# Kernel tuning notes

Hardware: AMD Instinct MI355X
Metric: run time of the kernel (lower is better)

The kernel has to match this reference:

```python
import jax, jax.numpy as jnp
import numpy as np

N_HEAD, D_HEAD = 10, 38
D_MODEL, D_INNER = 380, 900
QLEN, BSZ = 1024, 4
MIN_LEN, MAX_LEN = -1024, 1024
EPS = 1e-5
SCALE = 1.0 / D_HEAD ** 0.5


def _ln(x, g, b):
    m = x.mean(-1, keepdims=True)
    v = ((x - m) ** 2).mean(-1, keepdims=True)
    return (x - m) / jnp.sqrt(v + EPS) * g + b


def setup_inputs() -> dict:
    key = jax.random.key(0)
    ks = jax.random.split(key, 10)
    s = 0.02
    w = jax.random.normal(ks[0], (QLEN, BSZ, D_MODEL), jnp.float32)
    # sinusoidal relative position embeddings over positions max_len .. min_len
    pos = jnp.arange(MAX_LEN, MIN_LEN - 1, -1, dtype=jnp.float32)  # [rlen]
    inv_freq = 1.0 / (10000.0 ** (jnp.arange(0, D_MODEL, 2, dtype=jnp.float32) / D_MODEL))
    sin_inp = pos[:, None] * inv_freq[None, :]
    r = jnp.concatenate([jnp.sin(sin_inp), jnp.cos(sin_inp)], axis=-1)  # [rlen, d_model]
    # causal mask, True = attend; layout [qlen, klen, bsz]
    attn_mask = jnp.broadcast_to(jnp.tril(jnp.ones((QLEN, QLEN), bool))[:, :, None], (QLEN, QLEN, BSZ))
    attn_relpos = jax.random.randint(ks[1], (BSZ, QLEN, QLEN), MIN_LEN, MAX_LEN + 1).astype(jnp.int32)
    return {
        'w': w,
        'r': r,
        'r_w_bias': s * jax.random.normal(ks[2], (N_HEAD, D_HEAD), jnp.float32),
        'r_r_bias': s * jax.random.normal(ks[3], (N_HEAD, D_HEAD), jnp.float32),
        'qkv_w': s * jax.random.normal(ks[4], (3 * N_HEAD * D_HEAD, D_MODEL), jnp.float32),
        'r_w': s * jax.random.normal(ks[5], (N_HEAD * D_HEAD, D_MODEL), jnp.float32),
        'o_w': s * jax.random.normal(ks[6], (D_MODEL, N_HEAD * D_HEAD), jnp.float32),
        'ln1_g': jnp.ones(D_MODEL, jnp.float32), 'ln1_b': jnp.zeros(D_MODEL, jnp.float32),
        'ff_w1': s * jax.random.normal(ks[7], (D_INNER, D_MODEL), jnp.float32),
        'ff_b1': jnp.zeros(D_INNER, jnp.float32),
        'ff_w2': s * jax.random.normal(ks[8], (D_MODEL, D_INNER), jnp.float32),
        'ff_b2': jnp.zeros(D_MODEL, jnp.float32),
        'ln2_g': jnp.ones(D_MODEL, jnp.float32), 'ln2_b': jnp.zeros(D_MODEL, jnp.float32),
        'attn_mask': attn_mask,
        'attn_relpos': attn_relpos,
        'min_len': MIN_LEN,
        'max_len': MAX_LEN,
    }


def reference(w, r, r_w_bias, r_r_bias, qkv_w, r_w, o_w, ln1_g, ln1_b,
              ff_w1, ff_b1, ff_w2, ff_b2, ln2_g, ln2_b,
              attn_mask, attn_relpos, min_len, max_len):
    qlen, bsz, _ = w.shape
    # qkv projection (no mems, post-lnorm)
    heads = jnp.einsum('ibm,hm->ibh', w, qkv_w)  # [q, b, 3*nh*dh]
    q, k, v = jnp.split(heads, 3, axis=-1)
    q = q.reshape(qlen, bsz, N_HEAD, D_HEAD)
    k = k.reshape(qlen, bsz, N_HEAD, D_HEAD)
    v = v.reshape(qlen, bsz, N_HEAD, D_HEAD)
    rk = (r @ r_w.T).reshape(-1, N_HEAD, D_HEAD)  # [rlen, nh, dh]
    # content score AC and position score BD (Transformer-XL)
    AC = jnp.einsum('ibnd,jbnd->ijbn', q + r_w_bias, k)   # [q, k, b, n]
    BD = jnp.einsum('ibnd,jnd->ijbn', q + r_r_bias, rk)   # [q, rlen, b, n]
    # gather-based relative position indexing (attn_relpos path)
    idx = (max_len - jnp.clip(attn_relpos, min_len, max_len)).transpose(1, 2, 0)  # [q, k, b]
    idx4 = jnp.broadcast_to(idx[..., None], idx.shape + (N_HEAD,))
    BD = jnp.take_along_axis(BD, idx4, axis=1)            # [q, k, b, n]
    score = (AC + BD) * SCALE
    score = jnp.where(attn_mask[:, :, :, None], score, -jnp.inf)
    prob = jax.nn.softmax(score, axis=1)
    vec = jnp.einsum('ijbn,jbnd->ibnd', prob, v).reshape(qlen, bsz, N_HEAD * D_HEAD)
    attn_out = vec @ o_w.T
    out = _ln(w + attn_out, ln1_g, ln1_b)
    # position-wise FF, post-lnorm
    core = jax.nn.relu(out @ ff_w1.T + ff_b1) @ ff_w2.T + ff_b2
    return _ln(out + core, ln2_g, ln2_b)
```

## Files before the change

kernel.cpp:

```cpp
#include <hip/hip_runtime.h>
#include <math.h>

#define QLEN 1024
#define BSZ 4
#define NH 10
#define DH 38
#define DM 380
#define DI 900
#define H3 1140
#define RLEN 2049
#define RLP 2112
#define RLD 2052
#define SCALE 0.16222142113076254f

typedef unsigned short ushortt;
typedef unsigned char uchar;
typedef __attribute__((ext_vector_type(8))) short short8;
typedef __attribute__((ext_vector_type(4))) float float4v;

__device__ __forceinline__ float bf2f(ushortt u) {
    return __uint_as_float(((unsigned int)u) << 16);
}
__device__ __forceinline__ ushortt f2bf(float f) {
    unsigned int u = __float_as_uint(f);
    u += 0x7fffu + ((u >> 16) & 1u);
    return (ushortt)(u >> 16);
}
__device__ __forceinline__ uchar f2e4m3(float f) {
    unsigned u = __float_as_uint(f);
    unsigned s = (u >> 24) & 0x80u;
    unsigned b = u & 0x7fffffffu;
    b += 0x7FFFFu + ((b >> 20) & 1u);
    int E = (int)(b >> 23) - 120;
    if (E <= 0) return (uchar)s;
    if (E > 15 || (E == 15 && ((b >> 20) & 7u) > 6u)) return (uchar)(s | 0x7Eu);
    return (uchar)(s | ((unsigned)E << 3) | ((b >> 20) & 7u));
}
__device__ __forceinline__ float e4m32f(uchar v) {
    unsigned s = ((unsigned)(v & 0x80u)) << 24;
    int E = (v >> 3) & 15; unsigned m = v & 7u;
    if (E == 0) return __uint_as_float(s);
    return __uint_as_float(s | ((unsigned)(E + 120) << 23) | (m << 20));
}

__device__ __forceinline__ void convseg(const float* src, ushortt* dst,
                                        int R, int C, int Rp, int Cp,
                                        int tid0, int stride) {
    const int total = Rp * Cp;
    for (int i = tid0; i < total; i += stride) {
        int r = i / Cp, c = i - r * Cp;
        float v = (r < R && c < C) ? src[(size_t)r * C + c] : 0.f;
        dst[i] = f2bf(v);
    }
}

__global__ __launch_bounds__(256)
void prep_all(const float* __restrict__ w,    ushortt* __restrict__ w_bf,
              const float* __restrict__ qkv,  ushortt* __restrict__ qkv_bf,
              const float* __restrict__ r,    ushortt* __restrict__ r_bf,
              const float* __restrict__ rw,   ushortt* __restrict__ rw_bf,
              const float* __restrict__ ow,   ushortt* __restrict__ ow_bf,
              const float* __restrict__ f1,   ushortt* __restrict__ f1_bf,
              const float* __restrict__ f2,   ushortt* __restrict__ f2_bf,
              ushortt* __restrict__ qw_bf, ushortt* __restrict__ Kb, ushortt* __restrict__ Vb,
              ushortt* __restrict__ qr_bf, ushortt* __restrict__ rk_bf,
              ushortt* __restrict__ vec) {
    const int stride = gridDim.x * 256;
    const int tid0 = blockIdx.x * 256 + threadIdx.x;
    convseg(w,   w_bf,   4096, DM, 4096, 384, tid0, stride);
    convseg(qkv, qkv_bf, H3,   DM, 1152, 384, tid0, stride);
    convseg(r,   r_bf,   RLEN, DM, 2176, 384, tid0, stride);
    convseg(rw,  rw_bf,  DM,   DM, 384,  384, tid0, stride);
    convseg(ow,  ow_bf,  DM,   DM, 384,  384, tid0, stride);
    convseg(f1,  f1_bf,  DI,   DM, 960,  384, tid0, stride);
    convseg(f2,  f2_bf,  DM,   DI, 384,  928, tid0, stride);
    for (int i = tid0; i < BSZ * NH * 1024 * 2; i += stride) {
        size_t idx = (size_t)(i >> 1) * 40 + 38 + (i & 1);
        qw_bf[idx] = 0; Kb[idx] = 0; Vb[idx] = 0;
    }
    for (int i = tid0; i < 4096 * 4; i += stride)
        vec[(size_t)(i >> 2) * 384 + 380 + (i & 3)] = 0;
    for (int i = tid0; i < BSZ * NH * 1024 * 26; i += stride) {
        int row = i / 26, c = 38 + i % 26;
        qr_bf[(size_t)row * 64 + c] = 0;
    }
    for (int i = tid0; i < NH * RLP * 26; i += stride) {
        int row = i / 26, c = 38 + i % 26;
        rk_bf[(size_t)row * 64 + c] = 0;
    }
    for (int i = tid0; i < NH * 63 * 64; i += stride) {
        int n = i / (63 * 64), rem = i % (63 * 64);
        rk_bf[((size_t)n * RLP + RLEN + rem / 64) * 64 + rem % 64] = 0;
    }
}

template<int EPI>
__global__ __launch_bounds__(256)
void gemm_mfma(const ushortt* __restrict__ A, const ushortt* __restrict__ B,
               const float* __restrict__ bias, void* __restrict__ Cout,
               int M, int N, int Kpp, int ldc,
               const float* __restrict__ bias2, float* __restrict__ out2,
               float* __restrict__ out3, float* __restrict__ out4) {
    __shared__ __align__(16) ushortt As[128 * 32];
    __shared__ __align__(16) ushortt Bs[64 * 32];
    const int tid = threadIdx.x;
    const int wid = tid >> 6, lane = tid & 63;
    const int bRow = blockIdx.y * 128, bCol = blockIdx.x * 64;

    float4v acc[2][4];
    const float4v zz = {0.f, 0.f, 0.f, 0.f};
    #pragma unroll
    for (int m = 0; m < 2; ++m)
        #pragma unroll
        for (int n = 0; n < 4; ++n) acc[m][n] = zz;

    const int arow = tid >> 1, acol = (tid & 1) * 16;
    const int brow = tid >> 2, bcol = (tid & 3) * 8;
    const int fr = lane & 15, kg = lane >> 4;

    for (int k0 = 0; k0 < Kpp; k0 += 32) {
        const ushortt* ag = A + (size_t)(bRow + arow) * Kpp + k0 + acol;
        float4v a0 = *(const float4v*)ag;
        float4v a1 = *(const float4v*)(ag + 8);
        const ushortt* bg = B + (size_t)(bCol + brow) * Kpp + k0 + bcol;
        float4v b0 = *(const float4v*)bg;
        __syncthreads();
        *(float4v*)&As[arow * 32 + acol] = a0;
        *(float4v*)&As[arow * 32 + acol + 8] = a1;
        *(float4v*)&Bs[brow * 32 + bcol] = b0;
        __syncthreads();

        short8 bf[4];
        #pragma unroll
        for (int n = 0; n < 4; ++n)
            bf[n] = *(const short8*)&Bs[(n * 16 + fr) * 32 + kg * 8];
        #pragma unroll
        for (int m = 0; m < 2; ++m) {
            short8 af = *(const short8*)&As[(wid * 32 + m * 16 + fr) * 32 + kg * 8];
            #pragma unroll
            for (int n = 0; n < 4; ++n)
                acc[m][n] = __builtin_amdgcn_mfma_f32_16x16x32_bf16(af, bf[n], acc[m][n], 0, 0, 0);
        }
    }

    #pragma unroll
    for (int m = 0; m < 2; ++m)
        #pragma unroll
        for (int n = 0; n < 4; ++n)
            #pragma unroll
            for (int j = 0; j < 4; ++j) {
                const int row = bRow + wid * 32 + m * 16 + (lane >> 4) * 4 + j;
                const int col = bCol + n * 16 + (lane & 15);
                const float v = acc[m][n][j];
                if (EPI == 0) {
                    if (row < M && col < N) ((float*)Cout)[(size_t)row * ldc + col] = v;
                } else if (EPI == 3) {
                    if (row < M && col < 928) {
                        float h = (col < DI) ? fmaxf(v + bias[col], 0.f) : 0.f;
                        ((ushortt*)Cout)[(size_t)row * 928 + col] = f2bf(h);
                    }
                } else if (EPI == 4) {
                    if (row < M && col < N) ((float*)Cout)[(size_t)row * ldc + col] = v + bias[col];
                } else if (EPI == 5) {
                    if (col < H3) {
                        int part = col / 380;
                        int c = col - part * 380;
                        int nh = c / 38, d = c - nh * 38;
                        int q = row >> 2, b2 = row & 3;
                        size_t i40 = (((size_t)b2 * NH + nh) * 1024 + q) * 40 + d;
                        size_t i64 = (((size_t)b2 * NH + nh) * 1024 + q) * 64 + d;
                        if (part == 0) {
                            ((ushortt*)Cout)[i40] = f2bf(v + bias[c]);
                            ((ushortt*)out2)[i64] = f2bf(v + bias2[c]);
                        } else if (part == 1) ((ushortt*)out3)[i40] = f2bf(v);
                        else ((ushortt*)out4)[i40] = f2bf(v);
                    }
                } else {
                    if (row < RLEN && col < DM) {
                        int nh = col / 38, d = col - nh * 38;
                        ((ushortt*)Cout)[((size_t)nh * RLP + row) * 64 + d] = f2bf(v);
                    }
                }
            }
}

__global__ __launch_bounds__(256)
void bd_gemm(const ushortt* __restrict__ qr, const ushortt* __restrict__ rk,
             uchar* __restrict__ BD, int bofs, int nb) {
    __shared__ __align__(16) ushortt As[64][72];
    __shared__ __align__(16) ushortt Bs[32][72];
    __shared__ __align__(16) uchar Call[64 * 32 * 10];
    const int bid = blockIdx.x;
    const int xcd = bid & 7, t = bid >> 3;
    const int gl = t / 65, jt = t - gl * 65;
    const int G = gl * 8 + xcd;
    const int lb = G >> 4, qt = G & 15;
    const int tid = threadIdx.x;
    const int wid = tid >> 6, lane = tid & 63;
    const int j0 = jt * 32, q0 = qt * 64;
    const int fr = lane & 15, kg = lane >> 4;
    const int jcount = min(32, RLEN - j0);

    for (int n = 0; n < NH; ++n) {
        const ushortt* Ab = qr + (((size_t)(bofs + lb) * NH + n) * 1024 + q0) * 64;
        const ushortt* Bb = rk + ((size_t)n * RLP + j0) * 64;
        __syncthreads();
        {
            int rr = tid >> 2, cc = (tid & 3) * 16;
            *(float4v*)&As[rr][cc] = *(const float4v*)(Ab + (size_t)rr * 64 + cc);
            *(float4v*)&As[rr][cc + 8] = *(const float4v*)(Ab + (size_t)rr * 64 + cc + 8);
            int br = tid >> 3, bc = (tid & 7) * 8;
            *(float4v*)&Bs[br][bc] = *(const float4v*)(Bb + (size_t)br * 64 + bc);
        }
        __syncthreads();
        float4v acc[2] = {{0.f,0.f,0.f,0.f},{0.f,0.f,0.f,0.f}};
        #pragma unroll
        for (int ks = 0; ks < 64; ks += 32) {
            short8 af = *(const short8*)&As[wid * 16 + fr][ks + kg * 8];
            #pragma unroll
            for (int c = 0; c < 2; ++c) {
                short8 bfr = *(const short8*)&Bs[c * 16 + fr][ks + kg * 8];
                acc[c] = __builtin_amdgcn_mfma_f32_16x16x32_bf16(af, bfr, acc[c], 0, 0, 0);
            }
        }
        #pragma unroll
        for (int c = 0; c < 2; ++c)
            #pragma unroll
            for (int jj = 0; jj < 4; ++jj) {
                int rq = wid * 16 + (lane >> 4) * 4 + jj;
                int cj = c * 16 + (lane & 15);
                Call[(rq * 32 + cj) * 10 + n] = f2e4m3(acc[c][jj]);
            }
    }
    __syncthreads();
    if (jcount == 32) {
        const unsigned* Cdw = (const unsigned*)Call;
        unsigned* G2 = (unsigned*)BD;
        for (int idx = tid; idx < 64 * 80; idx += 256) {
            int rr = idx / 80, rem = idx - rr * 80;
            size_t gdw = (((size_t)(lb * 1024 + q0 + rr) * RLD + j0) * 10) >> 2;
            G2[gdw + rem] = Cdw[rr * 80 + rem];
        }
    } else {
        for (int idx = tid; idx < 64 * 10; idx += 256) {
            int rr = idx / 10, n2 = idx - rr * 10;
            BD[((size_t)(lb * 1024 + q0 + rr) * RLD + j0) * 10 + n2] = Call[rr * 320 + n2];
        }
    }
}

__global__ __launch_bounds__(256)
void attn7(const ushortt* __restrict__ qwb, const ushortt* __restrict__ Kp,
           const ushortt* __restrict__ Vp, const uchar* __restrict__ BD,
           const int* __restrict__ relpos,
           ushortt* __restrict__ op, float2* __restrict__ ml, int b0, int nb) {
    const int bid = blockIdx.x;
    const int xcd = bid & 7, t = bid >> 3;
    const int gl = t / 10, n = t - gl * 10;
    const int G = gl * 8 + xcd;
    int qc, lb, s;
    {
        const int c3 = 32 * nb, c2 = 24 * nb, c1 = 16 * nb;
        if (G < c3)                { qc = 31 - G / (4 * nb); int r2 = G % (4 * nb); lb = r2 >> 2; s = r2 & 3; }
        else if (G < c3 + c2)      { int l2 = G - c3; qc = 23 - l2 / (3 * nb); int r2 = l2 % (3 * nb); lb = r2 / 3; s = r2 % 3; }
        else if (G < c3 + c2 + c1) { int l2 = G - c3 - c2; qc = 15 - l2 / (2 * nb); int r2 = l2 % (2 * nb); lb = r2 >> 1; s = r2 & 1; }
        else                       { int l2 = G - c3 - c2 - c1; qc = 7 - l2 / nb; lb = l2 % nb; s = 0; }
    }
    const int ns = (qc >> 3) + 1;
    const int qbase = qc * 32;
    const int b = b0 + lb;
    const int tid = threadIdx.x;
    const int wid = tid >> 6, lane = tid & 63;
    const int row = tid >> 3, kg = tid & 7;
    const int qi = qbase + row;
    const size_t bn = (size_t)b * NH + n;
    const size_t prow = ((size_t)s * (BSZ * NH) + bn) * 1024 + qi;
    const int ntiles = (qbase + 95) >> 6;

    __shared__ __align__(16) ushortt KtL[64 * 48];
    __shared__ __align__(16) ushortt VtL[64 * 40];
    __shared__ __align__(16) ushortt qwL[32 * 48];
    __shared__ __align__(16) ushortt sL[32 * 66];

    const ushortt* Kbase = Kp + bn * 1024 * 40;
    const ushortt* Vbase = Vp + bn * 1024 * 40;
    const int fr = lane & 15;
    const int kg8 = (lane >> 4) * 8;
    const bool kgz = (lane >> 4) == 0;
    const short8 z8 = {0, 0, 0, 0, 0, 0, 0, 0};

    for (int e = tid; e < 160; e += 256) {
        int rr = e / 5, cc = (e % 5) * 8;
        *(short8*)&qwL[rr * 48 + cc] = *(const short8*)(qwb + (bn * 1024 + qbase + rr) * 40 + cc);
    }
    float o[5] = {0.f, 0.f, 0.f, 0.f, 0.f};
    float mrun = -INFINITY, lrun = 0.f;
    const int* rp = relpos + ((size_t)b * QLEN + qi) * QLEN;
    const uchar* bdrow = BD + ((size_t)(lb * 1024 + qi)) * (RLD * 10) + n;

    for (int kt = s; kt < ntiles; kt += ns) {
        const int k0 = kt * 64;
        __syncthreads();
        for (int e = tid; e < 320; e += 256) {
            int rr = e / 5, cc = (e % 5) * 8;
            *(short8*)&KtL[rr * 48 + cc] = *(const short8*)(Kbase + (size_t)(k0 + rr) * 40 + cc);
        }
        for (int e = tid; e < 320; e += 256)
            ((short8*)VtL)[e] = ((const short8*)(Vbase + (size_t)k0 * 40))[e];
        __syncthreads();

        int jv[8];
        #pragma unroll
        for (int ss = 0; ss < 8; ++ss) {
            const int kk = k0 + kg + ss * 8;
            int j = -1;
            if (kk <= qi) {
                int rpv = rp[kk];
                rpv = rpv < -1024 ? -1024 : (rpv > 1024 ? 1024 : rpv);
                j = 1024 - rpv;
            }
            jv[ss] = j;
        }
        float bdv[8];
        #pragma unroll
        for (int ss = 0; ss < 8; ++ss)
            bdv[ss] = (jv[ss] >= 0) ? e4m32f(bdrow[(size_t)jv[ss] * 10]) : 0.f;

        {
            const int mt = wid >> 1, ctb = (wid & 1) * 2;
            short8 a0 = *(const short8*)&qwL[(mt * 16 + fr) * 48 + kg8];
            short8 a1 = kgz ? *(const short8*)&qwL[(mt * 16 + fr) * 48 + 32] : z8;
            #pragma unroll
            for (int c = 0; c < 2; ++c) {
                const int ct = ctb + c;
                short8 b0f = *(const short8*)&KtL[(ct * 16 + fr) * 48 + kg8];
                short8 b1f = kgz ? *(const short8*)&KtL[(ct * 16 + fr) * 48 + 32] : z8;
                float4v acc = {0.f, 0.f, 0.f, 0.f};
                acc = __builtin_amdgcn_mfma_f32_16x16x32_bf16(a0, b0f, acc, 0, 0, 0);
                acc = __builtin_amdgcn_mfma_f32_16x16x32_bf16(a1, b1f, acc, 0, 0, 0);
                #pragma unroll
                for (int j = 0; j < 4; ++j)
                    sL[(mt * 16 + (lane >> 4) * 4 + j) * 66 + ct * 16 + fr] = f2bf(acc[j]);
            }
        }
        __syncthreads();

        float sarr[8];
        float pmax = -INFINITY;
        #pragma unroll
        for (int ss = 0; ss < 8; ++ss) {
            float sv = -INFINITY;
            if (jv[ss] >= 0)
                sv = (bf2f(sL[row * 66 + kg + ss * 8]) + bdv[ss]) * SCALE;
            sarr[ss] = sv;
            pmax = fmaxf(pmax, sv);
        }
        pmax = fmaxf(pmax, __shfl_xor(pmax, 1, 64));
        pmax = fmaxf(pmax, __shfl_xor(pmax, 2, 64));
        pmax = fmaxf(pmax, __shfl_xor(pmax, 4, 64));
        const float nm = fmaxf(mrun, pmax);
        const float corr = __expf(mrun - nm);
        float psum = 0.f;
        ushortt* prw = sL + row * 66;
        #pragma unroll
        for (int ss = 0; ss < 8; ++ss) {
            float p = __expf(sarr[ss] - nm);
            psum += p;
            prw[kg + ss * 8] = f2bf(p);
        }
        psum += __shfl_xor(psum, 1, 64);
        psum += __shfl_xor(psum, 2, 64);
        psum += __shfl_xor(psum, 4, 64);
        lrun = lrun * corr + psum;
        mrun = nm;
        #pragma unroll
        for (int jj = 0; jj < 5; ++jj) o[jj] *= corr;
        int kmax = qi - k0 + 1; if (kmax > 64) kmax = 64;
        #pragma unroll 4
        for (int k = 0; k < kmax; ++k) {
            float p = bf2f(prw[k]);
            const ushortt* vr = VtL + k * 40;
            uint2 v4u = *(const uint2*)(vr + 4 * kg);
            o[0] += p * bf2f((ushortt)(v4u.x & 0xffff));
            o[1] += p * bf2f((ushortt)(v4u.x >> 16));
            o[2] += p * bf2f((ushortt)(v4u.y & 0xffff));
            o[3] += p * bf2f((ushortt)(v4u.y >> 16));
            o[4] += p * bf2f(vr[32 + kg]);
        }
    }
    ushortt* oprow = op + prow * 40;
    #pragma unroll
    for (int jj = 0; jj < 4; ++jj) oprow[4 * kg + jj] = f2bf(o[jj]);
    oprow[32 + kg] = f2bf(o[4]);
    if (kg == 0) ml[prow] = make_float2(mrun, lrun);
}

__global__ __launch_bounds__(256)
void attn_combine(const ushortt* __restrict__ op, const float2* __restrict__ ml,
                  ushortt* __restrict__ vec) {
    const int idx = blockIdx.x * 256 + threadIdx.x;
    if (idx >= BSZ * NH * 1024 * 38) return;
    const int d = idx % 38;
    const int rh = idx / 38;
    const int q = rh & 1023;
    const int bn = rh >> 10;
    const int b = bn / NH, n = bn - b * NH;
    const int ns = ((q >> 5) >> 3) + 1;
    const size_t stride = (size_t)BSZ * NH * 1024;
    float M = -INFINITY;
    float2 mv[4];
    for (int sp = 0; sp < ns; ++sp) {
        mv[sp] = ml[sp * stride + rh];
        M = fmaxf(M, mv[sp].x);
    }
    float l = 0.f, o = 0.f;
    for (int sp = 0; sp < ns; ++sp) {
        float w = __expf(mv[sp].x - M);
        l += mv[sp].y * w;
        o += bf2f(op[(sp * stride + rh) * 40 + d]) * w;
    }
    vec[((size_t)q * BSZ + b) * 384 + (size_t)n * 38 + d] = f2bf(o / l);
}

template<bool WRITE_BF>
__global__ __launch_bounds__(256)
void ln_kernel(const float* __restrict__ x1, const float* __restrict__ x2,
               const float* __restrict__ g, const float* __restrict__ bb,
               float* __restrict__ outf, ushortt* __restrict__ outbf) {
    const int row = blockIdx.x;
    const float* p1 = x1 + (size_t)row * DM;
    const float* p2 = x2 + (size_t)row * DM;
    __shared__ float xb[DM];
    __shared__ float red[256];
    const int tid = threadIdx.x;
    float s = 0.f;
    for (int i = tid; i < DM; i += 256) { float v = p1[i] + p2[i]; xb[i] = v; s += v; }
    red[tid] = s; __syncthreads();
    for (int st = 128; st > 0; st >>= 1) { if (tid < st) red[tid] += red[tid + st]; __syncthreads(); }
    const float mean = red[0] / DM;
    __syncthreads();
    float s2 = 0.f;
    for (int i = tid; i < DM; i += 256) { float d = xb[i] - mean; s2 += d * d; }
    red[tid] = s2; __syncthreads();
    for (int st = 128; st > 0; st >>= 1) { if (tid < st) red[tid] += red[tid + st]; __syncthreads(); }
    const float rstd = rsqrtf(red[0] / DM + 1e-5f);
    for (int i = tid; i < (WRITE_BF ? 384 : DM); i += 256) {
        float v = 0.f;
        if (i < DM) {
            v = (xb[i] - mean) * rstd * g[i] + bb[i];
            outf[(size_t)row * DM + i] = v;
        }
        if (WRITE_BF) outbf[(size_t)row * 384 + i] = f2bf(i < DM ? v : 0.f);
    }
}

extern "C" void kernel_launch(void* const* d_in, const int* in_sizes, int n_in,
                              void* d_out, int out_size, void* d_ws, size_t ws_size,
                              hipStream_t stream) {
    const float* w     = (const float*)d_in[0];
    const float* r     = (const float*)d_in[1];
    const float* rwb   = (const float*)d_in[2];
    const float* rrb   = (const float*)d_in[3];
    const float* qkv_w = (const float*)d_in[4];
    const float* r_w   = (const float*)d_in[5];
    const float* o_w   = (const float*)d_in[6];
    const float* ln1g  = (const float*)d_in[7];
    const float* ln1b  = (const float*)d_in[8];
    const float* ffw1  = (const float*)d_in[9];
    const float* ffb1  = (const float*)d_in[10];
    const float* ffw2  = (const float*)d_in[11];
    const float* ffb2  = (const float*)d_in[12];
    const float* ln2g  = (const float*)d_in[13];
    const float* ln2b  = (const float*)d_in[14];
    const int*   relpos = (const int*)d_in[16];
    float* out = (float*)d_out;

    char* cur = (char*)d_ws;
    auto alloc = [&](size_t bytes) { char* p = cur; cur += (bytes + 255) & ~(size_t)255; return p; };
    ushortt* w_bf    = (ushortt*)alloc((size_t)4096 * 384 * 2);
    ushortt* qkv_bf  = (ushortt*)alloc((size_t)1152 * 384 * 2);
    ushortt* r_bf    = (ushortt*)alloc((size_t)2176 * 384 * 2);
    ushortt* rw_bf   = (ushortt*)alloc((size_t)384 * 384 * 2);
    ushortt* ow_bf   = (ushortt*)alloc((size_t)384 * 384 * 2);
    ushortt* f1_bf   = (ushortt*)alloc((size_t)960 * 384 * 2);
    ushortt* f2_bf   = (ushortt*)alloc((size_t)384 * 928 * 2);
    ushortt* qw_bf   = (ushortt*)alloc((size_t)BSZ * NH * 1024 * 40 * 2);
    ushortt* K_bf    = (ushortt*)alloc((size_t)BSZ * NH * 1024 * 40 * 2);
    ushortt* V_bf    = (ushortt*)alloc((size_t)BSZ * NH * 1024 * 40 * 2);
    ushortt* qr_bf   = (ushortt*)alloc((size_t)BSZ * NH * 1024 * 64 * 2);
    ushortt* rk_bf   = (ushortt*)alloc((size_t)NH * RLP * 64 * 2);
    ushortt* vec_bf  = (ushortt*)alloc((size_t)4096 * 384 * 2);
    ushortt* out1_bf = (ushortt*)alloc((size_t)4096 * 384 * 2);
    ushortt* h1_bf   = (ushortt*)alloc((size_t)4096 * 928 * 2);
    float*   attnf   = (float*)alloc((size_t)4096 * DM * 4);
    float*   out1f   = (float*)alloc((size_t)4096 * DM * 4);
    float*   core    = (float*)alloc((size_t)4096 * DM * 4);

    ushortt* op_part = (ushortt*)attnf;
    float2*  ml_part = (float2*)((char*)attnf + (size_t)4 * BSZ * NH * 1024 * 40 * 2);

    const size_t bd_b_bytes = (size_t)1024 * RLD * 10;
    uchar* BD = (uchar*)alloc(bd_b_bytes * BSZ);
    bool full = ((size_t)(cur - (char*)d_ws) <= ws_size);
    if (!full) { cur = (char*)BD; BD = (uchar*)alloc(bd_b_bytes); }

    auto cgrid = [](size_t total) { return dim3((unsigned)((total + 255) / 256)); };
    prep_all<<<dim3(2048), 256, 0, stream>>>(w, w_bf, qkv_w, qkv_bf, r, r_bf,
                                             r_w, rw_bf, o_w, ow_bf, ffw1, f1_bf, ffw2, f2_bf,
                                             qw_bf, K_bf, V_bf, qr_bf, rk_bf, vec_bf);

    gemm_mfma<5><<<dim3(18, 32), 256, 0, stream>>>(w_bf, qkv_bf, rwb, qw_bf, 4096, H3, 384, 0,
                                                   rrb, (float*)qr_bf, (float*)K_bf, (float*)V_bf);
    gemm_mfma<6><<<dim3(6, 17), 256, 0, stream>>>(r_bf, rw_bf, nullptr, rk_bf, RLEN, DM, 384, 0,
                                                  nullptr, nullptr, nullptr, nullptr);
    if (full) {
        bd_gemm<<<dim3(65 * 16 * BSZ), 256, 0, stream>>>(qr_bf, rk_bf, BD, 0, BSZ);
        attn7<<<dim3(3200), 256, 0, stream>>>(qw_bf, K_bf, V_bf, BD, relpos,
                                              op_part, ml_part, 0, BSZ);
    } else {
        for (int b = 0; b < BSZ; ++b) {
            bd_gemm<<<dim3(65 * 16), 256, 0, stream>>>(qr_bf, rk_bf, BD, b, 1);
            attn7<<<dim3(800), 256, 0, stream>>>(qw_bf, K_bf, V_bf, BD, relpos,
                                                 op_part, ml_part, b, 1);
        }
    }
    attn_combine<<<cgrid((size_t)BSZ * NH * 1024 * 38), 256, 0, stream>>>(op_part, ml_part, vec_bf);
    gemm_mfma<0><<<dim3(6, 32), 256, 0, stream>>>(vec_bf, ow_bf, nullptr, attnf, 4096, DM, 384, DM,
                                                  nullptr, nullptr, nullptr, nullptr);
    ln_kernel<true><<<4096, 256, 0, stream>>>(w, attnf, ln1g, ln1b, out1f, out1_bf);
    gemm_mfma<3><<<dim3(15, 32), 256, 0, stream>>>(out1_bf, f1_bf, ffb1, h1_bf, 4096, DI, 384, 928,
                                                   nullptr, nullptr, nullptr, nullptr);
    gemm_mfma<4><<<dim3(6, 32), 256, 0, stream>>>(h1_bf, f2_bf, ffb2, core, 4096, DM, 928, DM,
                                                  nullptr, nullptr, nullptr, nullptr);
    ln_kernel<false><<<4096, 256, 0, stream>>>(out1f, core, ln2g, ln2b, out, nullptr);
}
```

Baseline: 352.4 us.

## Enlarge attention query tile to 64 rows and rebalance split-K schedule

The attention kernel now processes 64 query rows per block instead of 32. Each thread owns 16 keys and 10 output dims, and each wave computes a full 16x64 score tile. This halves the block count and reuses every K/V tile load across twice as many queries, lowering global and LDS load traffic per query. The cost is more registers per thread, fewer blocks for load balancing, and a coarser split schedule, which the combine kernel is updated to match.

Measured after the change: 387.6 us. +10.0%, slower.

```diff
diff --git a/kernel.cpp b/kernel.cpp
--- a/kernel.cpp
+++ b/kernel.cpp
@@ -250,7 +250,7 @@
 }
 
 __global__ __launch_bounds__(256)
-void attn7(const ushortt* __restrict__ qwb, const ushortt* __restrict__ Kp,
+void attn8(const ushortt* __restrict__ qwb, const ushortt* __restrict__ Kp,
            const ushortt* __restrict__ Vp, const uchar* __restrict__ BD,
            const int* __restrict__ relpos,
            ushortt* __restrict__ op, float2* __restrict__ ml, int b0, int nb) {
@@ -260,27 +260,27 @@
     const int G = gl * 8 + xcd;
     int qc, lb, s;
     {
-        const int c3 = 32 * nb, c2 = 24 * nb, c1 = 16 * nb;
-        if (G < c3)                { qc = 31 - G / (4 * nb); int r2 = G % (4 * nb); lb = r2 >> 2; s = r2 & 3; }
-        else if (G < c3 + c2)      { int l2 = G - c3; qc = 23 - l2 / (3 * nb); int r2 = l2 % (3 * nb); lb = r2 / 3; s = r2 % 3; }
-        else if (G < c3 + c2 + c1) { int l2 = G - c3 - c2; qc = 15 - l2 / (2 * nb); int r2 = l2 % (2 * nb); lb = r2 >> 1; s = r2 & 1; }
-        else                       { int l2 = G - c3 - c2 - c1; qc = 7 - l2 / nb; lb = l2 % nb; s = 0; }
-    }
-    const int ns = (qc >> 3) + 1;
-    const int qbase = qc * 32;
+        const int c4 = 16 * nb, c3 = 12 * nb, c2 = 8 * nb;
+        if (G < c4)                { qc = 15 - G / (4 * nb); int r2 = G % (4 * nb); lb = r2 >> 2; s = r2 & 3; }
+        else if (G < c4 + c3)      { int g2 = G - c4; qc = 11 - g2 / (3 * nb); int r2 = g2 % (3 * nb); lb = r2 / 3; s = r2 % 3; }
+        else if (G < c4 + c3 + c2) { int g2 = G - c4 - c3; qc = 7 - g2 / (2 * nb); int r2 = g2 % (2 * nb); lb = r2 >> 1; s = r2 & 1; }
+        else                       { int g2 = G - c4 - c3 - c2; qc = 3 - g2 / nb; lb = g2 % nb; s = 0; }
+    }
+    const int ns = (qc >> 2) + 1;
+    const int ntiles = qc + 1;
+    const int qbase = qc * 64;
     const int b = b0 + lb;
     const int tid = threadIdx.x;
     const int wid = tid >> 6, lane = tid & 63;
-    const int row = tid >> 3, kg = tid & 7;
+    const int row = tid >> 2, kg = tid & 3;
     const int qi = qbase + row;
     const size_t bn = (size_t)b * NH + n;
     const size_t prow = ((size_t)s * (BSZ * NH) + bn) * 1024 + qi;
-    const int ntiles = (qbase + 95) >> 6;
 
     __shared__ __align__(16) ushortt KtL[64 * 48];
     __shared__ __align__(16) ushortt VtL[64 * 40];
-    __shared__ __align__(16) ushortt qwL[32 * 48];
-    __shared__ __align__(16) ushortt sL[32 * 66];
+    __shared__ __align__(16) ushortt qwL[64 * 48];
+    __shared__ __align__(16) ushortt sL[64 * 66];
 
     const ushortt* Kbase = Kp + bn * 1024 * 40;
     const ushortt* Vbase = Vp + bn * 1024 * 40;
@@ -289,11 +289,13 @@
     const bool kgz = (lane >> 4) == 0;
     const short8 z8 = {0, 0, 0, 0, 0, 0, 0, 0};
 
-    for (int e = tid; e < 160; e += 256) {
+    for (int e = tid; e < 320; e += 256) {
         int rr = e / 5, cc = (e % 5) * 8;
         *(short8*)&qwL[rr * 48 + cc] = *(const short8*)(qwb + (bn * 1024 + qbase + rr) * 40 + cc);
     }
-    float o[5] = {0.f, 0.f, 0.f, 0.f, 0.f};
+    float o[10];
+    #pragma unroll
+    for (int i = 0; i < 10; ++i) o[i] = 0.f;
     float mrun = -INFINITY, lrun = 0.f;
     const int* rp = relpos + ((size_t)b * QLEN + qi) * QLEN;
     const uchar* bdrow = BD + ((size_t)(lb * 1024 + qi)) * (RLD * 10) + n;
@@ -309,30 +311,27 @@
             ((short8*)VtL)[e] = ((const short8*)(Vbase + (size_t)k0 * 40))[e];
         __syncthreads();
 
-        int jv[8];
-        #pragma unroll
-        for (int ss = 0; ss < 8; ++ss) {
-            const int kk = k0 + kg + ss * 8;
-            int j = -1;
+        float bdv[16];
+        unsigned vmask = 0;
+        #pragma unroll
+        for (int ss = 0; ss < 16; ++ss) {
+            const int kk = k0 + kg + ss * 4;
+            float bv = 0.f;
             if (kk <= qi) {
                 int rpv = rp[kk];
                 rpv = rpv < -1024 ? -1024 : (rpv > 1024 ? 1024 : rpv);
-                j = 1024 - rpv;
+                bv = e4m32f(bdrow[(size_t)(1024 - rpv) * 10]);
+                vmask |= 1u << ss;
             }
-            jv[ss] = j;
-        }
-        float bdv[8];
-        #pragma unroll
-        for (int ss = 0; ss < 8; ++ss)
-            bdv[ss] = (jv[ss] >= 0) ? e4m32f(bdrow[(size_t)jv[ss] * 10]) : 0.f;
+            bdv[ss] = bv;
+        }
 
         {
-            const int mt = wid >> 1, ctb = (wid & 1) * 2;
+            const int mt = wid;
             short8 a0 = *(const short8*)&qwL[(mt * 16 + fr) * 48 + kg8];
             short8 a1 = kgz ? *(const short8*)&qwL[(mt * 16 + fr) * 48 + 32] : z8;
             #pragma unroll
-            for (int c = 0; c < 2; ++c) {
-                const int ct = ctb + c;
+            for (int ct = 0; ct < 4; ++ct) {
                 short8 b0f = *(const short8*)&KtL[(ct * 16 + fr) * 48 + kg8];
                 short8 b1f = kgz ? *(const short8*)&KtL[(ct * 16 + fr) * 48 + 32] : z8;
                 float4v acc = {0.f, 0.f, 0.f, 0.f};
@@ -345,53 +344,50 @@
         }
         __syncthreads();
 
-        float sarr[8];
+        ushortt* prw = sL + row * 66;
         float pmax = -INFINITY;
         #pragma unroll
-        for (int ss = 0; ss < 8; ++ss) {
+        for (int ss = 0; ss < 16; ++ss) {
+            const int k = kg + ss * 4;
             float sv = -INFINITY;
-            if (jv[ss] >= 0)
-                sv = (bf2f(sL[row * 66 + kg + ss * 8]) + bdv[ss]) * SCALE;
-            sarr[ss] = sv;
+            if (vmask & (1u << ss))
+                sv = (bf2f(prw[k]) + bdv[ss]) * SCALE;
+            bdv[ss] = sv;
             pmax = fmaxf(pmax, sv);
         }
         pmax = fmaxf(pmax, __shfl_xor(pmax, 1, 64));
         pmax = fmaxf(pmax, __shfl_xor(pmax, 2, 64));
-        pmax = fmaxf(pmax, __shfl_xor(pmax, 4, 64));
         const float nm = fmaxf(mrun, pmax);
         const float corr = __expf(mrun - nm);
         float psum = 0.f;
-        ushortt* prw = sL + row * 66;
-        #pragma unroll
-        for (int ss = 0; ss < 8; ++ss) {
-            float p = __expf(sarr[ss] - nm);
+        #pragma unroll
+        for (int ss = 0; ss < 16; ++ss) {
+            float p = __expf(bdv[ss] - nm);
             psum += p;
-            prw[kg + ss * 8] = f2bf(p);
+            prw[kg + ss * 4] = f2bf(p);
         }
         psum += __shfl_xor(psum, 1, 64);
         psum += __shfl_xor(psum, 2, 64);
-        psum += __shfl_xor(psum, 4, 64);
         lrun = lrun * corr + psum;
         mrun = nm;
         #pragma unroll
-        for (int jj = 0; jj < 5; ++jj) o[jj] *= corr;
+        for (int i = 0; i < 10; ++i) o[i] *= corr;
         int kmax = qi - k0 + 1; if (kmax > 64) kmax = 64;
         #pragma unroll 4
         for (int k = 0; k < kmax; ++k) {
             float p = bf2f(prw[k]);
-            const ushortt* vr = VtL + k * 40;
-            uint2 v4u = *(const uint2*)(vr + 4 * kg);
-            o[0] += p * bf2f((ushortt)(v4u.x & 0xffff));
-            o[1] += p * bf2f((ushortt)(v4u.x >> 16));
-            o[2] += p * bf2f((ushortt)(v4u.y & 0xffff));
-            o[3] += p * bf2f((ushortt)(v4u.y >> 16));
-            o[4] += p * bf2f(vr[32 + kg]);
-        }
-    }
-    ushortt* oprow = op + prow * 40;
+            const unsigned* vp = (const unsigned*)(VtL + k * 40 + kg * 10);
+            #pragma unroll
+            for (int i = 0; i < 5; ++i) {
+                unsigned u = vp[i];
+                o[2 * i]     += p * bf2f((ushortt)(u & 0xffff));
+                o[2 * i + 1] += p * bf2f((ushortt)(u >> 16));
+            }
+        }
+    }
+    ushortt* oprow = op + prow * 40 + kg * 10;
     #pragma unroll
-    for (int jj = 0; jj < 4; ++jj) oprow[4 * kg + jj] = f2bf(o[jj]);
-    oprow[32 + kg] = f2bf(o[4]);
+    for (int i = 0; i < 10; ++i) oprow[i] = f2bf(o[i]);
     if (kg == 0) ml[prow] = make_float2(mrun, lrun);
 }
 
@@ -405,7 +401,7 @@
     const int q = rh & 1023;
     const int bn = rh >> 10;
     const int b = bn / NH, n = bn - b * NH;
-    const int ns = ((q >> 5) >> 3) + 1;
+    const int ns = ((q >> 6) >> 2) + 1;
     const size_t stride = (size_t)BSZ * NH * 1024;
     float M = -INFINITY;
     float2 mv[4];
@@ -515,12 +511,12 @@
                                                   nullptr, nullptr, nullptr, nullptr);
     if (full) {
         bd_gemm<<<dim3(65 * 16 * BSZ), 256, 0, stream>>>(qr_bf, rk_bf, BD, 0, BSZ);
-        attn7<<<dim3(3200), 256, 0, stream>>>(qw_bf, K_bf, V_bf, BD, relpos,
+        attn8<<<dim3(1600), 256, 0, stream>>>(qw_bf, K_bf, V_bf, BD, relpos,
                                               op_part, ml_part, 0, BSZ);
     } else {
         for (int b = 0; b < BSZ; ++b) {
             bd_gemm<<<dim3(65 * 16), 256, 0, stream>>>(qr_bf, rk_bf, BD, b, 1);
-            attn7<<<dim3(800), 256, 0, stream>>>(qw_bf, K_bf, V_bf, BD, relpos,
+            attn8<<<dim3(400), 256, 0, stream>>>(qw_bf, K_bf, V_bf, BD, relpos,
                                                  op_part, ml_part, b, 1);
         }
     }
```
